# Optimization experiments

Measured on AMD Instinct MI355X. Metric: run time of the kernel, lower is better.

The kernel has to match this reference:

```python
import jax, jax.numpy as jnp
import numpy as np

DIM = 1024
NUM_HEADS = 16
HEAD_DIM = DIM // NUM_HEADS


def setup_inputs() -> dict:
    key = jax.random.key(0)
    ks = jax.random.split(key, 5)
    B, T = 2, 2048
    x = jax.random.normal(ks[0], (B, T, DIM), dtype=jnp.float32)
    s = 1.0 / np.sqrt(DIM)
    W_qkv = jax.random.normal(ks[1], (DIM, 3 * DIM), dtype=jnp.float32) * s
    b_qkv = jnp.zeros((3 * DIM,), dtype=jnp.float32)
    W_out = jax.random.normal(ks[2], (DIM, DIM), dtype=jnp.float32) * s
    b_out = jnp.zeros((DIM,), dtype=jnp.float32)
    return {"x": x, "W_qkv": W_qkv, "b_qkv": b_qkv, "W_out": W_out, "b_out": b_out}


def reference(x, W_qkv, b_qkv, W_out, b_out):
    B, T, D = x.shape
    H, Hd = NUM_HEADS, HEAD_DIM
    qkv = x @ W_qkv + b_qkv                       # [B,T,3D]
    qkv = qkv.reshape(B, T, 3, H, Hd)
    q = jnp.transpose(qkv[:, :, 0], (0, 2, 1, 3))  # [B,H,T,Hd]
    k = jnp.transpose(qkv[:, :, 1], (0, 2, 1, 3))
    v = jnp.transpose(qkv[:, :, 2], (0, 2, 1, 3))
    att = jnp.einsum('bhqd,bhkd->bhqk', q, k) / np.sqrt(Hd)  # [B,H,T,T]
    causal = jnp.tril(jnp.ones((T, T), dtype=bool))
    att = jnp.where(causal[None, None], att, -jnp.inf)
    att = jax.nn.softmax(att, axis=-1)
    out = jnp.einsum('bhqk,bhkd->bhqd', att, v)   # [B,H,T,Hd]
    out = jnp.transpose(out, (0, 2, 1, 3)).reshape(B, T, D)
    return out @ W_out + b_out
```

## Files before the change

kernel.cpp:

```cpp
#include <hip/hip_runtime.h>
#include <hip/hip_bf16.h>

typedef unsigned short u16;
typedef __attribute__((ext_vector_type(8))) short short8;
typedef __attribute__((ext_vector_type(4))) float f32x4;
typedef __attribute__((ext_vector_type(4))) unsigned short u16x4;

#define LOG2E 1.44269504088896340736f


__device__ __forceinline__ void gl_lds16(const void* g, void* l) {
  __builtin_amdgcn_global_load_lds(
      (__attribute__((address_space(1))) void*)g,
      (__attribute__((address_space(3))) void*)l, 16, 0, 0);
}

__device__ __forceinline__ u16 f2bf(float f) {
  union { float f; unsigned int i; } v;
  v.f = f;
  unsigned int r = v.i + 0x7fffu + ((v.i >> 16) & 1u);
  return (u16)(r >> 16);
}

__device__ __forceinline__ unsigned int pack_bf2(float lo, float hi) {
  union { __hip_bfloat162 h2; unsigned int u; } c;
  c.h2 = __float22bfloat162_rn(make_float2(lo, hi));
  return c.u;
}


__global__ __launch_bounds__(256) void cvt_bf16(const float4* __restrict__ in,
                                                u16x4* __restrict__ out) {
  int i = blockIdx.x * 256 + threadIdx.x;
  float4 v = in[i];
  u16x4 o;
  o.x = f2bf(v.x); o.y = f2bf(v.y); o.z = f2bf(v.z); o.w = f2bf(v.w);
  out[i] = o;
}


__global__ __launch_bounds__(256) void transpose_cvt(
    const float* __restrict__ W, u16* __restrict__ WT, int K, int N) {
  __shared__ u16 t[64][65];
  int r0 = blockIdx.y * 64, c0 = blockIdx.x * 64;
  int tx = threadIdx.x & 63, ty = threadIdx.x >> 6;
  for (int r = ty; r < 64; r += 4)
    t[r][tx] = f2bf(W[(size_t)(r0 + r) * N + c0 + tx]);
  __syncthreads();
  for (int r = ty; r < 64; r += 4)
    WT[(size_t)(c0 + r) * K + r0 + tx] = t[tx][r];
}


template <bool OUT_F32>
__global__ __launch_bounds__(256) void gemm_bt_kernel(
    const u16* __restrict__ A, const u16* __restrict__ Bt,
    const float* __restrict__ bias, void* __restrict__ Cout,
    int M, int N, int K) {
  __shared__ u16 As[128 * 32];
  __shared__ u16 Bs[128 * 32];
  int tid = threadIdx.x;
  int w = tid >> 6, lane = tid & 63, l15 = lane & 15, quad = lane >> 4;
  int m0 = blockIdx.y * 128, n0 = blockIdx.x * 128;
  int wm = (w & 1) * 64, wn = (w >> 1) * 64;

  f32x4 acc[4][4];
#pragma unroll
  for (int i = 0; i < 4; ++i)
#pragma unroll
    for (int j = 0; j < 4; ++j) {
      f32x4 z = {0.f, 0.f, 0.f, 0.f};
      acc[i][j] = z;
    }

  int srow = lane >> 2;
  int scol = (lane & 3) * 8;

  for (int kt = 0; kt < K; kt += 32) {
    __syncthreads();
#pragma unroll
    for (int i = 0; i < 4; ++i) {
      int c = w * 4 + i;
      if (c < 8) {
        int row = m0 + c * 16 + srow;
        gl_lds16(A + (size_t)row * K + kt + scol, As + c * 512);
      } else {
        int cc = c - 8;
        int row = n0 + cc * 16 + srow;
        gl_lds16(Bt + (size_t)row * K + kt + scol, Bs + cc * 512);
      }
    }
    __syncthreads();

    short8 af[4], bf[4];
#pragma unroll
    for (int i = 0; i < 4; ++i)
      af[i] = *(const short8*)(As + (wm + i * 16 + l15) * 32 + quad * 8);
#pragma unroll
    for (int j = 0; j < 4; ++j)
      bf[j] = *(const short8*)(Bs + (wn + j * 16 + l15) * 32 + quad * 8);
#pragma unroll
    for (int i = 0; i < 4; ++i)
#pragma unroll
      for (int j = 0; j < 4; ++j)
        acc[i][j] = __builtin_amdgcn_mfma_f32_16x16x32_bf16(af[i], bf[j],
                                                            acc[i][j], 0, 0, 0);
  }

  float bv[4];
#pragma unroll
  for (int j = 0; j < 4; ++j) bv[j] = bias[n0 + wn + j * 16 + l15];
#pragma unroll
  for (int i = 0; i < 4; ++i)
#pragma unroll
    for (int j = 0; j < 4; ++j) {
      int col = n0 + wn + j * 16 + l15;
#pragma unroll
      for (int r = 0; r < 4; ++r) {
        int row = m0 + wm + i * 16 + quad * 4 + r;
        float val = acc[i][j][r] + bv[j];
        if (OUT_F32)
          ((float*)Cout)[(size_t)row * N + col] = val;
        else
          ((u16*)Cout)[(size_t)row * N + col] = f2bf(val);
      }
    }
}


__global__ __launch_bounds__(256) void flash_kernel(const u16* __restrict__ qkv,
                                                    u16* __restrict__ att) {
  __shared__ unsigned int Ks[2][64 * 32];
  __shared__ unsigned int Vt[2][64 * 32];
  __shared__ unsigned int Ps[4 * 16 * 32];

  int tid = threadIdx.x, w = tid >> 6, lane = tid & 63;
  int l15 = lane & 15, quad = lane >> 4;
  int bx = blockIdx.x;
  int p = bx >> 5, bh = bx & 31, b = bh >> 4, h = bh & 15;
  const int qi[2] = {31 - p, p};
  const int kmax = qi[0];

  const u16* base = qkv + (size_t)b * 2048 * 3072 + h * 64;
  const u16* kb = base + 1024;
  const u16* vb = base + 2048;

  short8 onesf;
#pragma unroll
  for (int j = 0; j < 8; ++j) onesf[j] = (l15 == 0) ? (short)0x3F80 : (short)0;

  short8 aq[2][2];
#pragma unroll
  for (int t = 0; t < 2; ++t) {
    const u16* qrow = base + (size_t)(qi[t] * 64 + w * 16 + l15) * 3072;
#pragma unroll
    for (int ss = 0; ss < 2; ++ss)
      aq[t][ss] = *(const short8*)(qrow + ss * 32 + quad * 8);
  }

  const int krow = tid >> 3, kc16 = (tid & 7) * 8;
  const int vpr = tid >> 3, vd0 = (tid & 7) * 8;

  uint4 kr0 = *(const uint4*)(kb + (size_t)krow * 3072 + kc16);
  uint4 kr1 = *(const uint4*)(kb + (size_t)(krow + 32) * 3072 + kc16);
  uint4 vr0 = *(const uint4*)(vb + (size_t)(2 * vpr) * 3072 + vd0);
  uint4 vr1 = *(const uint4*)(vb + (size_t)(2 * vpr + 1) * 3072 + vd0);
  {
    *(uint4*)&Ks[0][32 * krow + ((4 * (tid & 7)) ^ ((krow & 7) << 2))] = kr0;
    int r1 = krow + 32;
    *(uint4*)&Ks[0][32 * r1 + ((4 * (tid & 7)) ^ ((r1 & 7) << 2))] = kr1;
    const u16* av = (const u16*)&vr0;
    const u16* bvp = (const u16*)&vr1;
#pragma unroll
    for (int j = 0; j < 8; ++j) {
      int d = vd0 + j;
      Vt[0][32 * d + (vpr ^ ((j ^ (tid & 7)) << 2))] =
          (unsigned int)av[j] | ((unsigned int)bvp[j] << 16);
    }
  }
  kr0 = *(const uint4*)(kb + (size_t)(64 + krow) * 3072 + kc16);
  kr1 = *(const uint4*)(kb + (size_t)(64 + krow + 32) * 3072 + kc16);
  vr0 = *(const uint4*)(vb + (size_t)(64 + 2 * vpr) * 3072 + vd0);
  vr1 = *(const uint4*)(vb + (size_t)(64 + 2 * vpr + 1) * 3072 + vd0);

  f32x4 o[2][5];
#pragma unroll
  for (int t = 0; t < 2; ++t)
#pragma unroll
    for (int jd = 0; jd < 5; ++jd) {
      f32x4 z = {0.f, 0.f, 0.f, 0.f};
      o[t][jd] = z;
    }

  unsigned int* Pw = Ps + w * 512;
  const int psw = (l15 & 7) << 2;
  const float kscale = 0.125f * LOG2E;
  const float fshift = 16.0f;

  for (int kt = 0; kt <= kmax; ++kt) {
    __syncthreads();
    if (kt < kmax) {
      int bufw = (kt + 1) & 1;
      *(uint4*)&Ks[bufw][32 * krow + ((4 * (tid & 7)) ^ ((krow & 7) << 2))] = kr0;
      int r1 = krow + 32;
      *(uint4*)&Ks[bufw][32 * r1 + ((4 * (tid & 7)) ^ ((r1 & 7) << 2))] = kr1;
      const u16* av = (const u16*)&vr0;
      const u16* bvp = (const u16*)&vr1;
#pragma unroll
      for (int j = 0; j < 8; ++j) {
        int d = vd0 + j;
        Vt[bufw][32 * d + (vpr ^ ((j ^ (tid & 7)) << 2))] =
            (unsigned int)av[j] | ((unsigned int)bvp[j] << 16);
      }
    }
    if (kt + 2 <= kmax) {
      int k0n = (kt + 2) * 64;
      kr0 = *(const uint4*)(kb + (size_t)(k0n + krow) * 3072 + kc16);
      kr1 = *(const uint4*)(kb + (size_t)(k0n + krow + 32) * 3072 + kc16);
      vr0 = *(const uint4*)(vb + (size_t)(k0n + 2 * vpr) * 3072 + vd0);
      vr1 = *(const uint4*)(vb + (size_t)(k0n + 2 * vpr + 1) * 3072 + vd0);
    }
    const unsigned int* Kb = Ks[kt & 1];
    const unsigned int* Vb = Vt[kt & 1];

#pragma unroll
    for (int t = 0; t < 2; ++t) {
      if (kt > qi[t]) continue;

      f32x4 s[4];
#pragma unroll
      for (int jn = 0; jn < 4; ++jn) {
        f32x4 z = {0.f, 0.f, 0.f, 0.f};
        s[jn] = z;
      }
#pragma unroll
      for (int ss = 0; ss < 2; ++ss)
#pragma unroll
        for (int jn = 0; jn < 4; ++jn) {
          int row = jn * 16 + l15;
          short8 bk = *(const short8*)&Kb[32 * row + ((16 * ss + 4 * quad) ^
                                                      ((row & 7) << 2))];
          s[jn] = __builtin_amdgcn_mfma_f32_16x16x32_bf16(bk, aq[t][ss], s[jn],
                                                          0, 0, 0);
        }

      bool diag = (kt == qi[t]);
      int qloc = w * 16 + l15;
#pragma unroll
      for (int jn = 0; jn < 4; ++jn) {
        float pv[4];
#pragma unroll
        for (int r = 0; r < 4; ++r) {
          float sv = s[jn][r];
          if (diag && (jn * 16 + quad * 4 + r > qloc)) sv = -1e30f;
          pv[r] = exp2f(fmaf(sv, kscale, -fshift));
        }
        uint2 dd = make_uint2(pack_bf2(pv[0], pv[1]), pack_bf2(pv[2], pv[3]));
        *(uint2*)&Pw[32 * l15 + (((jn << 3) + (quad << 1)) ^ psw)] = dd;
      }

#pragma unroll
      for (int ss = 0; ss < 2; ++ss) {
        short8 pf = *(const short8*)&Pw[32 * l15 + (((ss << 4) + (quad << 2)) ^
                                                    psw)];
#pragma unroll
        for (int jd = 0; jd < 4; ++jd) {
          int vrow = jd * 16 + l15;
          int f = (vrow & 7) ^ ((vrow >> 3) & 7);
          short8 bvv = *(const short8*)&Vb[32 * vrow +
                                           (((ss << 4) + (quad << 2)) ^ (f << 2))];
          o[t][jd] =
              __builtin_amdgcn_mfma_f32_16x16x32_bf16(bvv, pf, o[t][jd], 0, 0, 0);
        }
        o[t][4] =
            __builtin_amdgcn_mfma_f32_16x16x32_bf16(onesf, pf, o[t][4], 0, 0, 0);
      }
    }
  }

#pragma unroll
  for (int t = 0; t < 2; ++t) {
    float lr = __shfl(o[t][4][0], l15, 64);
    float inv = 1.f / lr;
    size_t row = (size_t)b * 2048 + qi[t] * 64 + w * 16 + l15;
    u16* orow = att + row * 1024 + h * 64 + quad * 4;
#pragma unroll
    for (int jd = 0; jd < 4; ++jd) {
      uint2 dd = make_uint2(pack_bf2(o[t][jd][0] * inv, o[t][jd][1] * inv),
                            pack_bf2(o[t][jd][2] * inv, o[t][jd][3] * inv));
      *(uint2*)(orow + jd * 16) = dd;
    }
  }
}


extern "C" void kernel_launch(void* const* d_in, const int* in_sizes, int n_in,
                              void* d_out, int out_size, void* d_ws,
                              size_t ws_size, hipStream_t stream) {
  const float* x = (const float*)d_in[0];
  const float* Wqkv = (const float*)d_in[1];
  const float* bqkv = (const float*)d_in[2];
  const float* Wout = (const float*)d_in[3];
  const float* bout = (const float*)d_in[4];
  float* out = (float*)d_out;

  char* ws = (char*)d_ws;
  u16* WqkvT = (u16*)(ws);
  u16* WoutT = (u16*)(ws + 6291456);
  u16* qkv = (u16*)(ws + 8388608);
  u16* attn = (u16*)(ws + 33554432);
  u16* xb = (u16*)(ws + 41943040);

  cvt_bf16<<<4096, 256, 0, stream>>>((const float4*)x, (u16x4*)xb);
  transpose_cvt<<<dim3(48, 16), 256, 0, stream>>>(Wqkv, WqkvT, 1024, 3072);
  transpose_cvt<<<dim3(16, 16), 256, 0, stream>>>(Wout, WoutT, 1024, 1024);
  gemm_bt_kernel<false><<<dim3(24, 32), 256, 0, stream>>>(
      xb, WqkvT, bqkv, (void*)qkv, 4096, 3072, 1024);
  flash_kernel<<<512, 256, 0, stream>>>(qkv, attn);
  gemm_bt_kernel<true><<<dim3(8, 32), 256, 0, stream>>>(
      attn, WoutT, bout, (void*)out, 4096, 1024, 1024);
}
```

Measured before the change: 197.5 us.

## Split flash attention KV loop across two wave-halves; narrow output GEMM tile

After: 232.3 us. 17.6% more time.

```diff
diff --git a/kernel.cpp b/kernel.cpp
--- a/kernel.cpp
+++ b/kernel.cpp
@@ -52,23 +52,26 @@
 }
 
 
-template <bool OUT_F32>
+template <bool OUT_F32, int BN>
 __global__ __launch_bounds__(256) void gemm_bt_kernel(
     const u16* __restrict__ A, const u16* __restrict__ Bt,
     const float* __restrict__ bias, void* __restrict__ Cout,
     int M, int N, int K) {
+  constexpr int NBJ = BN / 32;
+  constexpr int CHUNKS = 8 + BN / 16;
+  constexpr int PER_W = CHUNKS / 4;
   __shared__ u16 As[128 * 32];
-  __shared__ u16 Bs[128 * 32];
+  __shared__ u16 Bs[BN * 32];
   int tid = threadIdx.x;
   int w = tid >> 6, lane = tid & 63, l15 = lane & 15, quad = lane >> 4;
-  int m0 = blockIdx.y * 128, n0 = blockIdx.x * 128;
-  int wm = (w & 1) * 64, wn = (w >> 1) * 64;
-
-  f32x4 acc[4][4];
+  int m0 = blockIdx.y * 128, n0 = blockIdx.x * BN;
+  int wm = (w & 1) * 64, wn = (w >> 1) * (BN / 2);
+
+  f32x4 acc[4][NBJ];
 #pragma unroll
   for (int i = 0; i < 4; ++i)
 #pragma unroll
-    for (int j = 0; j < 4; ++j) {
+    for (int j = 0; j < NBJ; ++j) {
       f32x4 z = {0.f, 0.f, 0.f, 0.f};
       acc[i][j] = z;
     }
@@ -79,8 +82,8 @@
   for (int kt = 0; kt < K; kt += 32) {
     __syncthreads();
 #pragma unroll
-    for (int i = 0; i < 4; ++i) {
-      int c = w * 4 + i;
+    for (int i = 0; i < PER_W; ++i) {
+      int c = w * PER_W + i;
       if (c < 8) {
         int row = m0 + c * 16 + srow;
         gl_lds16(A + (size_t)row * K + kt + scol, As + c * 512);
@@ -92,28 +95,28 @@
     }
     __syncthreads();
 
-    short8 af[4], bf[4];
+    short8 af[4], bf[NBJ];
 #pragma unroll
     for (int i = 0; i < 4; ++i)
       af[i] = *(const short8*)(As + (wm + i * 16 + l15) * 32 + quad * 8);
 #pragma unroll
-    for (int j = 0; j < 4; ++j)
+    for (int j = 0; j < NBJ; ++j)
       bf[j] = *(const short8*)(Bs + (wn + j * 16 + l15) * 32 + quad * 8);
 #pragma unroll
     for (int i = 0; i < 4; ++i)
 #pragma unroll
-      for (int j = 0; j < 4; ++j)
+      for (int j = 0; j < NBJ; ++j)
         acc[i][j] = __builtin_amdgcn_mfma_f32_16x16x32_bf16(af[i], bf[j],
                                                             acc[i][j], 0, 0, 0);
   }
 
-  float bv[4];
-#pragma unroll
-  for (int j = 0; j < 4; ++j) bv[j] = bias[n0 + wn + j * 16 + l15];
+  float bv[NBJ];
+#pragma unroll
+  for (int j = 0; j < NBJ; ++j) bv[j] = bias[n0 + wn + j * 16 + l15];
 #pragma unroll
   for (int i = 0; i < 4; ++i)
 #pragma unroll
-    for (int j = 0; j < 4; ++j) {
+    for (int j = 0; j < NBJ; ++j) {
       int col = n0 + wn + j * 16 + l15;
 #pragma unroll
       for (int r = 0; r < 4; ++r) {
@@ -128,18 +131,20 @@
 }
 
 
-__global__ __launch_bounds__(256) void flash_kernel(const u16* __restrict__ qkv,
-                                                    u16* __restrict__ att) {
-  __shared__ unsigned int Ks[2][64 * 32];
-  __shared__ unsigned int Vt[2][64 * 32];
-  __shared__ unsigned int Ps[4 * 16 * 32];
-
-  int tid = threadIdx.x, w = tid >> 6, lane = tid & 63;
-  int l15 = lane & 15, quad = lane >> 4;
+__global__ __launch_bounds__(512, 4) void flash_kernel(
+    const u16* __restrict__ qkv, u16* __restrict__ att) {
+  __shared__ unsigned int SH[20480];
+
+  int tid = threadIdx.x;
+  int w = tid >> 6;
+  int half = w >> 2;
+  int wq = w & 3;
+  int lane = tid & 63, l15 = lane & 15, quad = lane >> 4;
   int bx = blockIdx.x;
   int p = bx >> 5, bh = bx & 31, b = bh >> 4, h = bh & 15;
   const int qi[2] = {31 - p, p};
   const int kmax = qi[0];
+  const int jmax = (kmax >> 1) + 1;
 
   const u16* base = qkv + (size_t)b * 2048 * 3072 + h * 64;
   const u16* kb = base + 1024;
@@ -152,36 +157,44 @@
   short8 aq[2][2];
 #pragma unroll
   for (int t = 0; t < 2; ++t) {
-    const u16* qrow = base + (size_t)(qi[t] * 64 + w * 16 + l15) * 3072;
+    const u16* qrow = base + (size_t)(qi[t] * 64 + wq * 16 + l15) * 3072;
 #pragma unroll
     for (int ss = 0; ss < 2; ++ss)
       aq[t][ss] = *(const short8*)(qrow + ss * 32 + quad * 8);
   }
 
-  const int krow = tid >> 3, kc16 = (tid & 7) * 8;
-  const int vpr = tid >> 3, vd0 = (tid & 7) * 8;
-
-  uint4 kr0 = *(const uint4*)(kb + (size_t)krow * 3072 + kc16);
-  uint4 kr1 = *(const uint4*)(kb + (size_t)(krow + 32) * 3072 + kc16);
-  uint4 vr0 = *(const uint4*)(vb + (size_t)(2 * vpr) * 3072 + vd0);
-  uint4 vr1 = *(const uint4*)(vb + (size_t)(2 * vpr + 1) * 3072 + vd0);
+  int ht = tid & 255;
+  const int krow = ht >> 3, h7 = ht & 7, kc16 = h7 * 8;
+  const int vpr = ht >> 3, vd0 = h7 * 8;
+
+  unsigned int* KsH = SH + half * 4096;
+  unsigned int* VtH = SH + 8192 + half * 4096;
+  unsigned int* Pw = SH + 16384 + w * 512;
+
+  uint4 kr0 = *(const uint4*)(kb + (size_t)(half * 64 + krow) * 3072 + kc16);
+  uint4 kr1 = *(const uint4*)(kb + (size_t)(half * 64 + krow + 32) * 3072 + kc16);
+  uint4 vr0 = *(const uint4*)(vb + (size_t)(half * 64 + 2 * vpr) * 3072 + vd0);
+  uint4 vr1 = *(const uint4*)(vb + (size_t)(half * 64 + 2 * vpr + 1) * 3072 + vd0);
   {
-    *(uint4*)&Ks[0][32 * krow + ((4 * (tid & 7)) ^ ((krow & 7) << 2))] = kr0;
+    *(uint4*)&KsH[32 * krow + ((4 * h7) ^ ((krow & 7) << 2))] = kr0;
     int r1 = krow + 32;
-    *(uint4*)&Ks[0][32 * r1 + ((4 * (tid & 7)) ^ ((r1 & 7) << 2))] = kr1;
+    *(uint4*)&KsH[32 * r1 + ((4 * h7) ^ ((r1 & 7) << 2))] = kr1;
     const u16* av = (const u16*)&vr0;
     const u16* bvp = (const u16*)&vr1;
 #pragma unroll
     for (int j = 0; j < 8; ++j) {
       int d = vd0 + j;
-      Vt[0][32 * d + (vpr ^ ((j ^ (tid & 7)) << 2))] =
+      VtH[32 * d + (vpr ^ ((j ^ h7) << 2))] =
           (unsigned int)av[j] | ((unsigned int)bvp[j] << 16);
     }
   }
-  kr0 = *(const uint4*)(kb + (size_t)(64 + krow) * 3072 + kc16);
-  kr1 = *(const uint4*)(kb + (size_t)(64 + krow + 32) * 3072 + kc16);
-  vr0 = *(const uint4*)(vb + (size_t)(64 + 2 * vpr) * 3072 + vd0);
-  vr1 = *(const uint4*)(vb + (size_t)(64 + 2 * vpr + 1) * 3072 + vd0);
+  {
+    int kn = (half + 2) * 64;
+    kr0 = *(const uint4*)(kb + (size_t)(kn + krow) * 3072 + kc16);
+    kr1 = *(const uint4*)(kb + (size_t)(kn + krow + 32) * 3072 + kc16);
+    vr0 = *(const uint4*)(vb + (size_t)(kn + 2 * vpr) * 3072 + vd0);
+    vr1 = *(const uint4*)(vb + (size_t)(kn + 2 * vpr + 1) * 3072 + vd0);
+  }
 
   f32x4 o[2][5];
 #pragma unroll
@@ -192,103 +205,128 @@
       o[t][jd] = z;
     }
 
-  unsigned int* Pw = Ps + w * 512;
   const int psw = (l15 & 7) << 2;
   const float kscale = 0.125f * LOG2E;
   const float fshift = 16.0f;
 
-  for (int kt = 0; kt <= kmax; ++kt) {
+  for (int j = 0; j < jmax; ++j) {
+    int kt = 2 * j + half;
     __syncthreads();
-    if (kt < kmax) {
-      int bufw = (kt + 1) & 1;
-      *(uint4*)&Ks[bufw][32 * krow + ((4 * (tid & 7)) ^ ((krow & 7) << 2))] = kr0;
+    if (kt + 2 <= kmax) {
+      unsigned int* KsB = KsH + ((j + 1) & 1) * 2048;
+      unsigned int* VtB = VtH + ((j + 1) & 1) * 2048;
+      *(uint4*)&KsB[32 * krow + ((4 * h7) ^ ((krow & 7) << 2))] = kr0;
       int r1 = krow + 32;
-      *(uint4*)&Ks[bufw][32 * r1 + ((4 * (tid & 7)) ^ ((r1 & 7) << 2))] = kr1;
+      *(uint4*)&KsB[32 * r1 + ((4 * h7) ^ ((r1 & 7) << 2))] = kr1;
       const u16* av = (const u16*)&vr0;
       const u16* bvp = (const u16*)&vr1;
 #pragma unroll
-      for (int j = 0; j < 8; ++j) {
-        int d = vd0 + j;
-        Vt[bufw][32 * d + (vpr ^ ((j ^ (tid & 7)) << 2))] =
-            (unsigned int)av[j] | ((unsigned int)bvp[j] << 16);
-      }
-    }
-    if (kt + 2 <= kmax) {
-      int k0n = (kt + 2) * 64;
-      kr0 = *(const uint4*)(kb + (size_t)(k0n + krow) * 3072 + kc16);
-      kr1 = *(const uint4*)(kb + (size_t)(k0n + krow + 32) * 3072 + kc16);
-      vr0 = *(const uint4*)(vb + (size_t)(k0n + 2 * vpr) * 3072 + vd0);
-      vr1 = *(const uint4*)(vb + (size_t)(k0n + 2 * vpr + 1) * 3072 + vd0);
-    }
-    const unsigned int* Kb = Ks[kt & 1];
-    const unsigned int* Vb = Vt[kt & 1];
-
+      for (int jj = 0; jj < 8; ++jj) {
+        int d = vd0 + jj;
+        VtB[32 * d + (vpr ^ ((jj ^ h7) << 2))] =
+            (unsigned int)av[jj] | ((unsigned int)bvp[jj] << 16);
+      }
+    }
+    if (kt + 4 <= kmax) {
+      int kn = (kt + 4) * 64;
+      kr0 = *(const uint4*)(kb + (size_t)(kn + krow) * 3072 + kc16);
+      kr1 = *(const uint4*)(kb + (size_t)(kn + krow + 32) * 3072 + kc16);
+      vr0 = *(const uint4*)(vb + (size_t)(kn + 2 * vpr) * 3072 + vd0);
+      vr1 = *(const uint4*)(vb + (size_t)(kn + 2 * vpr + 1) * 3072 + vd0);
+    }
+    if (kt <= kmax) {
+      const unsigned int* Kb = KsH + (j & 1) * 2048;
+      const unsigned int* Vb = VtH + (j & 1) * 2048;
+
+#pragma unroll
+      for (int t = 0; t < 2; ++t) {
+        if (kt > qi[t]) continue;
+
+        f32x4 s[4];
+#pragma unroll
+        for (int jn = 0; jn < 4; ++jn) {
+          f32x4 z = {0.f, 0.f, 0.f, 0.f};
+          s[jn] = z;
+        }
+#pragma unroll
+        for (int ss = 0; ss < 2; ++ss)
+#pragma unroll
+          for (int jn = 0; jn < 4; ++jn) {
+            int row = jn * 16 + l15;
+            short8 bk = *(const short8*)&Kb[32 * row + ((16 * ss + 4 * quad) ^
+                                                        ((row & 7) << 2))];
+            s[jn] = __builtin_amdgcn_mfma_f32_16x16x32_bf16(bk, aq[t][ss],
+                                                            s[jn], 0, 0, 0);
+          }
+
+        bool diag = (kt == qi[t]);
+        int qloc = wq * 16 + l15;
+#pragma unroll
+        for (int jn = 0; jn < 4; ++jn) {
+          float pv[4];
+#pragma unroll
+          for (int r = 0; r < 4; ++r) {
+            float sv = s[jn][r];
+            if (diag && (jn * 16 + quad * 4 + r > qloc)) sv = -1e30f;
+            pv[r] = exp2f(fmaf(sv, kscale, -fshift));
+          }
+          uint2 dd = make_uint2(pack_bf2(pv[0], pv[1]), pack_bf2(pv[2], pv[3]));
+          *(uint2*)&Pw[32 * l15 + (((jn << 3) + (quad << 1)) ^ psw)] = dd;
+        }
+
+#pragma unroll
+        for (int ss = 0; ss < 2; ++ss) {
+          short8 pf = *(const short8*)&Pw[32 * l15 +
+                                          (((ss << 4) + (quad << 2)) ^ psw)];
+#pragma unroll
+          for (int jd = 0; jd < 4; ++jd) {
+            int vrow = jd * 16 + l15;
+            int f = (vrow & 7) ^ ((vrow >> 3) & 7);
+            short8 bvv = *(const short8*)&Vb[32 * vrow + (((ss << 4) +
+                                                           (quad << 2)) ^
+                                                          (f << 2))];
+            o[t][jd] = __builtin_amdgcn_mfma_f32_16x16x32_bf16(bvv, pf,
+                                                               o[t][jd], 0, 0, 0);
+          }
+          o[t][4] = __builtin_amdgcn_mfma_f32_16x16x32_bf16(onesf, pf, o[t][4],
+                                                            0, 0, 0);
+        }
+      }
+    }
+  }
+
+  __syncthreads();
+  float* OM = (float*)SH;
+  float* LM = (float*)(SH + 8704);
+  if (half == 0) {
 #pragma unroll
     for (int t = 0; t < 2; ++t) {
-      if (kt > qi[t]) continue;
-
-      f32x4 s[4];
-#pragma unroll
-      for (int jn = 0; jn < 4; ++jn) {
-        f32x4 z = {0.f, 0.f, 0.f, 0.f};
-        s[jn] = z;
-      }
-#pragma unroll
-      for (int ss = 0; ss < 2; ++ss)
-#pragma unroll
-        for (int jn = 0; jn < 4; ++jn) {
-          int row = jn * 16 + l15;
-          short8 bk = *(const short8*)&Kb[32 * row + ((16 * ss + 4 * quad) ^
-                                                      ((row & 7) << 2))];
-          s[jn] = __builtin_amdgcn_mfma_f32_16x16x32_bf16(bk, aq[t][ss], s[jn],
-                                                          0, 0, 0);
-        }
-
-      bool diag = (kt == qi[t]);
-      int qloc = w * 16 + l15;
-#pragma unroll
-      for (int jn = 0; jn < 4; ++jn) {
-        float pv[4];
-#pragma unroll
-        for (int r = 0; r < 4; ++r) {
-          float sv = s[jn][r];
-          if (diag && (jn * 16 + quad * 4 + r > qloc)) sv = -1e30f;
-          pv[r] = exp2f(fmaf(sv, kscale, -fshift));
-        }
-        uint2 dd = make_uint2(pack_bf2(pv[0], pv[1]), pack_bf2(pv[2], pv[3]));
-        *(uint2*)&Pw[32 * l15 + (((jn << 3) + (quad << 1)) ^ psw)] = dd;
-      }
-
-#pragma unroll
-      for (int ss = 0; ss < 2; ++ss) {
-        short8 pf = *(const short8*)&Pw[32 * l15 + (((ss << 4) + (quad << 2)) ^
-                                                    psw)];
-#pragma unroll
-        for (int jd = 0; jd < 4; ++jd) {
-          int vrow = jd * 16 + l15;
-          int f = (vrow & 7) ^ ((vrow >> 3) & 7);
-          short8 bvv = *(const short8*)&Vb[32 * vrow +
-                                           (((ss << 4) + (quad << 2)) ^ (f << 2))];
-          o[t][jd] =
-              __builtin_amdgcn_mfma_f32_16x16x32_bf16(bvv, pf, o[t][jd], 0, 0, 0);
-        }
-        o[t][4] =
-            __builtin_amdgcn_mfma_f32_16x16x32_bf16(onesf, pf, o[t][4], 0, 0, 0);
-      }
-    }
-  }
-
-#pragma unroll
-  for (int t = 0; t < 2; ++t) {
-    float lr = __shfl(o[t][4][0], l15, 64);
-    float inv = 1.f / lr;
-    size_t row = (size_t)b * 2048 + qi[t] * 64 + w * 16 + l15;
-    u16* orow = att + row * 1024 + h * 64 + quad * 4;
-#pragma unroll
-    for (int jd = 0; jd < 4; ++jd) {
-      uint2 dd = make_uint2(pack_bf2(o[t][jd][0] * inv, o[t][jd][1] * inv),
-                            pack_bf2(o[t][jd][2] * inv, o[t][jd][3] * inv));
-      *(uint2*)(orow + jd * 16) = dd;
+      int q = wq * 16 + l15;
+#pragma unroll
+      for (int jd = 0; jd < 4; ++jd)
+        *(float4*)&OM[((size_t)t * 64 + q) * 68 + jd * 16 + quad * 4] =
+            *(float4*)&o[t][jd];
+      if (quad == 0) LM[t * 64 + q] = o[t][4][0];
+    }
+  }
+  __syncthreads();
+  if (half == 1) {
+#pragma unroll
+    for (int t = 0; t < 2; ++t) {
+      int q = wq * 16 + l15;
+      float lr = __shfl(o[t][4][0], l15, 64) + LM[t * 64 + q];
+      float inv = 1.f / lr;
+      size_t row = (size_t)b * 2048 + qi[t] * 64 + q;
+      u16* orow = att + row * 1024 + h * 64 + quad * 4;
+#pragma unroll
+      for (int jd = 0; jd < 4; ++jd) {
+        float4 pa = *(float4*)&OM[((size_t)t * 64 + q) * 68 + jd * 16 + quad * 4];
+        uint2 dd = make_uint2(pack_bf2((o[t][jd][0] + pa.x) * inv,
+                                       (o[t][jd][1] + pa.y) * inv),
+                              pack_bf2((o[t][jd][2] + pa.z) * inv,
+                                       (o[t][jd][3] + pa.w) * inv));
+        *(uint2*)(orow + jd * 16) = dd;
+      }
     }
   }
 }
@@ -314,9 +352,9 @@
   cvt_bf16<<<4096, 256, 0, stream>>>((const float4*)x, (u16x4*)xb);
   transpose_cvt<<<dim3(48, 16), 256, 0, stream>>>(Wqkv, WqkvT, 1024, 3072);
   transpose_cvt<<<dim3(16, 16), 256, 0, stream>>>(Wout, WoutT, 1024, 1024);
-  gemm_bt_kernel<false><<<dim3(24, 32), 256, 0, stream>>>(
+  gemm_bt_kernel<false, 128><<<dim3(24, 32), 256, 0, stream>>>(
       xb, WqkvT, bqkv, (void*)qkv, 4096, 3072, 1024);
-  flash_kernel<<<512, 256, 0, stream>>>(qkv, attn);
-  gemm_bt_kernel<true><<<dim3(8, 32), 256, 0, stream>>>(
+  flash_kernel<<<512, 512, 0, stream>>>(qkv, attn);
+  gemm_bt_kernel<true, 64><<<dim3(16, 32), 256, 0, stream>>>(
       attn, WoutT, bout, (void*)out, 4096, 1024, 1024);
 }
```
